# Kernel optimization log

Hardware: AMD Instinct MI355X
Metric: run time of the kernel (lower is better)

The kernel has to match this reference:

```python
import jax, jax.numpy as jnp
import numpy as np

H = 1024      # hidden_dim
S = 32768     # seq_len


def setup_inputs() -> dict:
    key = jax.random.key(0)
    k1, k2, k3, k4, k5 = jax.random.split(key, 5)
    hidden = jax.random.normal(k1, (1, 2 * H), dtype=jnp.float32)
    encoder_output = jax.random.normal(k2, (S, H), dtype=jnp.float32)
    # nn.Linear default init scale ~ 1/sqrt(fan_in)
    attn_w = jax.random.normal(k3, (H, 3 * H), dtype=jnp.float32) / np.sqrt(3 * H)
    attn_b = jax.random.normal(k4, (H,), dtype=jnp.float32) / np.sqrt(3 * H)
    v_w = jax.random.normal(k5, (1, H), dtype=jnp.float32) / np.sqrt(H)
    return {"hidden": hidden, "encoder_output": encoder_output,
            "attn_w": attn_w, "attn_b": attn_b, "v_w": v_w}


def reference(hidden, encoder_output, attn_w, attn_b, v_w):
    seq_len = encoder_output.shape[0]
    h_rep = jnp.broadcast_to(hidden, (seq_len, hidden.shape[1]))  # repeat(seq_len, 1)
    cat = jnp.concatenate([h_rep, encoder_output], axis=1)        # [S, 3H]
    energy = jnp.tanh(cat @ attn_w.T + attn_b)                    # [S, H]
    attention = (energy @ v_w.T).squeeze()                        # [S]
    return jax.nn.softmax(attention, axis=0)
```

## Files before the change

kernel.cpp:

```cpp
#include <hip/hip_runtime.h>
#include <hip/hip_bf16.h>

#define H  1024
#define S  32768
#define H2 2048
#define H3 3072

typedef __attribute__((ext_vector_type(8))) short bf16x8;
typedef __attribute__((ext_vector_type(4))) float f32x4;

__device__ __forceinline__ unsigned short f2bf(float f) {
    unsigned u = __float_as_uint(f);
    u += 0x7fffu + ((u >> 16) & 1u);
    return (unsigned short)(u >> 16);
}

__device__ __forceinline__ unsigned cvt_pk(float lo, float hi) {
    __hip_bfloat162 h = __float22bfloat162_rn(make_float2(lo, hi));
    unsigned u;
    __builtin_memcpy(&u, &h, 4);
    return u;
}

__device__ __forceinline__ float tanh_fast(float x) {
    float e = __expf(2.0f * x);
    return 1.0f - 2.0f / (e + 1.0f);
}

__device__ __forceinline__ void async_copy16(const void* g, void* l) {
    __builtin_amdgcn_global_load_lds(
        (const __attribute__((address_space(1))) unsigned int*)g,
        (__attribute__((address_space(3))) unsigned int*)l,
        16, 0, 0);
}

__global__ void prep_all(const float* __restrict__ enc, const float* __restrict__ attn_w,
                         const float* __restrict__ attn_b, const float* __restrict__ hidden,
                         unsigned short* __restrict__ ebf, unsigned short* __restrict__ w2b,
                         float* __restrict__ dvec, float* __restrict__ logits, int do_enc) {
    int b = blockIdx.x;
    if (b < 32) {
        ((float4*)logits)[b * 256 + threadIdx.x] = (float4){0.f, 0.f, 0.f, 0.f};
        return;
    }
    b -= 32;
    if (do_enc) {
        if (b < 32768) {
            size_t idx4 = (size_t)b * 256 + threadIdx.x;
            float4 f = ((const float4*)enc)[idx4];
            ushort4 u;
            u.x = f2bf(f.x); u.y = f2bf(f.y); u.z = f2bf(f.z); u.w = f2bf(f.w);
            ((ushort4*)ebf)[idx4] = u;
            return;
        }
        b -= 32768;
    }
    if (b < 1024) {
        int idx4 = b * 256 + threadIdx.x;
        int n = idx4 >> 8;
        int c = (idx4 & 255) * 4;
        float4 f = *(const float4*)(attn_w + (size_t)n * H3 + H2 + c);
        ushort4 u;
        u.x = f2bf(f.x); u.y = f2bf(f.y); u.z = f2bf(f.z); u.w = f2bf(f.w);
        *(ushort4*)(w2b + (size_t)n * H + c) = u;
        return;
    }
    b -= 1024;
    int wv = threadIdx.x >> 6, lane = threadIdx.x & 63;
    int row = b * 4 + wv;
    const float* wrow = attn_w + (size_t)row * H3;
    float s = 0.f;
    #pragma unroll
    for (int j = 0; j < 32; ++j) {
        int k = lane + j * 64;
        s += wrow[k] * hidden[k];
    }
    #pragma unroll
    for (int m = 1; m <= 32; m <<= 1) s += __shfl_xor(s, m);
    if (lane == 0) dvec[row] = s + attn_b[row];
}

__device__ __forceinline__ void epilogue(const f32x4 acc[4][4], const float* __restrict__ dvec,
                                         const float* __restrict__ vw, float* __restrict__ logits,
                                         int rowBlock, int colBlock, int waveM, int waveN,
                                         int quad, int l16) {
    float rowsum[4][4];
    #pragma unroll
    for (int mi = 0; mi < 4; ++mi)
        #pragma unroll
        for (int r = 0; r < 4; ++r) rowsum[mi][r] = 0.f;

    #pragma unroll
    for (int ni = 0; ni < 4; ++ni) {
        int colg = colBlock * 128 + waveN * 64 + ni * 16 + l16;
        float dv = dvec[colg];
        float vv = vw[colg];
        #pragma unroll
        for (int mi = 0; mi < 4; ++mi)
            #pragma unroll
            for (int r = 0; r < 4; ++r)
                rowsum[mi][r] += tanh_fast(acc[mi][ni][r] + dv) * vv;
    }

    #pragma unroll
    for (int mi = 0; mi < 4; ++mi)
        #pragma unroll
        for (int r = 0; r < 4; ++r) {
            float s = rowsum[mi][r];
            s += __shfl_xor(s, 1);
            s += __shfl_xor(s, 2);
            s += __shfl_xor(s, 4);
            s += __shfl_xor(s, 8);
            rowsum[mi][r] = s;
        }

    if (l16 == 0) {
        int rbase = rowBlock * 128 + waveM * 64 + quad * 4;
        #pragma unroll
        for (int mi = 0; mi < 4; ++mi)
            #pragma unroll
            for (int r = 0; r < 4; ++r)
                atomicAdd(&logits[rbase + mi * 16 + r], rowsum[mi][r]);
    }
}

__global__ __launch_bounds__(256, 2) void attn_gemm_fast(
        const unsigned short* __restrict__ ebf, const unsigned short* __restrict__ w2b,
        const float* __restrict__ dvec, const float* __restrict__ vw,
        float* __restrict__ logits) {
    __shared__ unsigned short Atile[128 * 64];
    __shared__ unsigned short Btile[128 * 64];

    const int tid = threadIdx.x;
    const int rowBlock = blockIdx.x & 255;
    const int colBlock = blockIdx.x >> 8;

    const int lane = tid & 63;
    const int wv = tid >> 6;
    const int waveM = wv >> 1, waveN = wv & 1;
    const int quad = lane >> 4, l16 = lane & 15;

    f32x4 acc[4][4];
    #pragma unroll
    for (int mi = 0; mi < 4; ++mi)
        #pragma unroll
        for (int ni = 0; ni < 4; ++ni)
            acc[mi][ni] = (f32x4){0.f, 0.f, 0.f, 0.f};

    const size_t aRow0 = (size_t)(rowBlock * 128) * H;
    const size_t bRow0 = (size_t)(colBlock * 128) * H;

    int srow[4], sk[4];
    #pragma unroll
    for (int p = 0; p < 4; ++p) {
        int c = p * 256 + tid;
        srow[p] = c >> 3;
        sk[p] = ((c & 7) ^ (srow[p] & 7)) * 8;
    }

    for (int kt = 0; kt < 16; ++kt) {
        const int k0 = kt * 64;

        #pragma unroll
        for (int p = 0; p < 4; ++p) {
            int c = p * 256 + tid;
            async_copy16(ebf + aRow0 + (size_t)srow[p] * H + k0 + sk[p],
                         (char*)Atile + (size_t)c * 16);
        }
        #pragma unroll
        for (int p = 0; p < 4; ++p) {
            int c = p * 256 + tid;
            async_copy16(w2b + bRow0 + (size_t)srow[p] * H + k0 + sk[p],
                         (char*)Btile + (size_t)c * 16);
        }

        __syncthreads();

        #pragma unroll
        for (int kk = 0; kk < 2; ++kk) {
            const int slot = ((kk * 4 + quad) ^ (l16 & 7)) * 16;
            bf16x8 af[4], bfr[4];
            #pragma unroll
            for (int i = 0; i < 4; ++i) {
                int ar = waveM * 64 + i * 16 + l16;
                int br = waveN * 64 + i * 16 + l16;
                af[i]  = *(const bf16x8*)((const char*)Atile + ar * 128 + slot);
                bfr[i] = *(const bf16x8*)((const char*)Btile + br * 128 + slot);
            }
            #pragma unroll
            for (int mi = 0; mi < 4; ++mi)
                #pragma unroll
                for (int ni = 0; ni < 4; ++ni)
                    acc[mi][ni] = __builtin_amdgcn_mfma_f32_16x16x32_bf16(
                        af[mi], bfr[ni], acc[mi][ni], 0, 0, 0);
        }

        __syncthreads();
    }

    epilogue(acc, dvec, vw, logits, rowBlock, colBlock, waveM, waveN, quad, l16);
}

__global__ __launch_bounds__(256, 2) void attn_gemm_fb(
        const float* __restrict__ enc, const unsigned short* __restrict__ w2b,
        const float* __restrict__ dvec, const float* __restrict__ vw,
        float* __restrict__ logits) {
    __shared__ unsigned short Atile[128 * 32];
    __shared__ unsigned short Btile[128 * 32];

    const int tid = threadIdx.x;
    const int rowBlock = blockIdx.x & 255;
    const int colBlock = blockIdx.x >> 8;

    const int lane = tid & 63;
    const int wv = tid >> 6;
    const int waveM = wv >> 1, waveN = wv & 1;
    const int quad = lane >> 4, l16 = lane & 15;

    f32x4 acc[4][4];
    #pragma unroll
    for (int mi = 0; mi < 4; ++mi)
        #pragma unroll
        for (int ni = 0; ni < 4; ++ni)
            acc[mi][ni] = (f32x4){0.f, 0.f, 0.f, 0.f};

    const int arow = tid >> 3;
    const int akc  = (tid & 7) * 4;
    const size_t encRowBase = (size_t)(rowBlock * 128) * H;

    const unsigned short* Abase = Atile + (waveM * 64 + l16) * 32 + quad * 8;
    const unsigned short* Bbase = Btile + (waveN * 64 + l16) * 32 + quad * 8;

    for (int kt = 0; kt < 32; ++kt) {
        const int k0 = kt * 32;
        #pragma unroll
        for (int p = 0; p < 2; ++p) {
            int c = p * 256 + tid;
            int n = c >> 2, kk = (c & 3) * 8;
            async_copy16(w2b + (size_t)(colBlock * 128 + n) * H + k0 + kk,
                         (char*)Btile + (size_t)c * 16);
        }
        float4 av[4];
        #pragma unroll
        for (int p = 0; p < 4; ++p)
            av[p] = *(const float4*)(enc + encRowBase + (size_t)(arow + p * 32) * H + k0 + akc);
        #pragma unroll
        for (int p = 0; p < 4; ++p) {
            uint2 u;
            u.x = cvt_pk(av[p].x, av[p].y);
            u.y = cvt_pk(av[p].z, av[p].w);
            *(uint2*)(Atile + (arow + p * 32) * 32 + akc) = u;
        }

        __syncthreads();

        bf16x8 af[4], bfr[4];
        #pragma unroll
        for (int i = 0; i < 4; ++i) {
            af[i]  = *(const bf16x8*)(Abase + i * 16 * 32);
            bfr[i] = *(const bf16x8*)(Bbase + i * 16 * 32);
        }
        #pragma unroll
        for (int mi = 0; mi < 4; ++mi)
            #pragma unroll
            for (int ni = 0; ni < 4; ++ni)
                acc[mi][ni] = __builtin_amdgcn_mfma_f32_16x16x32_bf16(
                    af[mi], bfr[ni], acc[mi][ni], 0, 0, 0);

        __syncthreads();
    }

    epilogue(acc, dvec, vw, logits, rowBlock, colBlock, waveM, waveN, quad, l16);
}

__global__ __launch_bounds__(1024) void softmax_k(float* __restrict__ x) {
    __shared__ float red[16];
    const int tid = threadIdx.x;
    const int lane = tid & 63, wv = tid >> 6;

    float v[32];
    float m = -1e30f;
    #pragma unroll
    for (int i = 0; i < 32; ++i) {
        v[i] = x[tid + (i << 10)];
        m = fmaxf(m, v[i]);
    }
    #pragma unroll
    for (int o = 1; o < 64; o <<= 1) m = fmaxf(m, __shfl_xor(m, o));
    if (lane == 0) red[wv] = m;
    __syncthreads();
    #pragma unroll
    for (int i = 0; i < 16; ++i) m = fmaxf(m, red[i]);
    __syncthreads();

    float s = 0.f;
    #pragma unroll
    for (int i = 0; i < 32; ++i) {
        v[i] = expf(v[i] - m);
        s += v[i];
    }
    #pragma unroll
    for (int o = 1; o < 64; o <<= 1) s += __shfl_xor(s, o);
    if (lane == 0) red[wv] = s;
    __syncthreads();
    float tot = 0.f;
    #pragma unroll
    for (int i = 0; i < 16; ++i) tot += red[i];
    float inv = 1.0f / tot;

    #pragma unroll
    for (int i = 0; i < 32; ++i) x[tid + (i << 10)] = v[i] * inv;
}

extern "C" void kernel_launch(void* const* d_in, const int* in_sizes, int n_in,
                              void* d_out, int out_size, void* d_ws, size_t ws_size,
                              hipStream_t stream) {
    const float* hidden = (const float*)d_in[0];
    const float* enc    = (const float*)d_in[1];
    const float* attn_w = (const float*)d_in[2];
    const float* attn_b = (const float*)d_in[3];
    const float* v_w    = (const float*)d_in[4];
    float* out = (float*)d_out;

    const size_t EBF_BYTES = (size_t)S * H * 2;
    const size_t W2_BYTES  = (size_t)H * H * 2;
    const bool fast = ws_size >= EBF_BYTES + W2_BYTES + 4096;

    if (fast) {
        unsigned short* ebf = (unsigned short*)d_ws;
        unsigned short* w2b = (unsigned short*)((char*)d_ws + EBF_BYTES);
        float* dvec = (float*)((char*)d_ws + EBF_BYTES + W2_BYTES);
        prep_all<<<dim3(32 + 32768 + 1024 + 256), dim3(256), 0, stream>>>(
            enc, attn_w, attn_b, hidden, ebf, w2b, dvec, out, 1);
        attn_gemm_fast<<<dim3(2048), dim3(256), 0, stream>>>(ebf, w2b, dvec, v_w, out);
    } else {
        unsigned short* w2b = (unsigned short*)d_ws;
        float* dvec = (float*)((char*)d_ws + W2_BYTES);
        prep_all<<<dim3(32 + 1024 + 256), dim3(256), 0, stream>>>(
            enc, attn_w, attn_b, hidden, nullptr, w2b, dvec, out, 0);
        attn_gemm_fb<<<dim3(2048), dim3(256), 0, stream>>>(enc, w2b, dvec, v_w, out);
    }
    softmax_k<<<dim3(1), dim3(1024), 0, stream>>>(out);
}
```

Baseline: 301.3 us.

## Load fp32 encoder tiles directly via async copy and convert to bf16 in registers

Removes the separate pass that converted the whole encoder output to bf16 in workspace. The GEMM now async-copies fp32 encoder tiles into a swizzled shared buffer and converts them to bf16 when building MFMA fragments. This saves the extra write and re-read of a 64MB bf16 copy. In exchange the GEMM reads twice as many A bytes per tile, which are re-read by all 8 column blocks. Shared memory use grows to 48KB per block and register-side conversion work is added.

```diff
diff --git a/kernel.cpp b/kernel.cpp
--- a/kernel.cpp
+++ b/kernel.cpp
@@ -124,11 +124,11 @@
     }
 }
 
-__global__ __launch_bounds__(256, 2) void attn_gemm_fast(
-        const unsigned short* __restrict__ ebf, const unsigned short* __restrict__ w2b,
+__global__ __launch_bounds__(256, 2) void attn_gemm_f32a(
+        const float* __restrict__ enc, const unsigned short* __restrict__ w2b,
         const float* __restrict__ dvec, const float* __restrict__ vw,
         float* __restrict__ logits) {
-    __shared__ unsigned short Atile[128 * 64];
+    __shared__ float Af[128 * 64];
     __shared__ unsigned short Btile[128 * 64];
 
     const int tid = threadIdx.x;
@@ -150,27 +150,34 @@
     const size_t aRow0 = (size_t)(rowBlock * 128) * H;
     const size_t bRow0 = (size_t)(colBlock * 128) * H;
 
-    int srow[4], sk[4];
+    int srA[8], skA[8];
+    #pragma unroll
+    for (int p = 0; p < 8; ++p) {
+        int c = p * 256 + tid;
+        srA[p] = c >> 4;
+        skA[p] = ((c & 15) ^ ((srA[p] & 7) << 1)) * 4;
+    }
+    int srB[4], skB[4];
     #pragma unroll
     for (int p = 0; p < 4; ++p) {
         int c = p * 256 + tid;
-        srow[p] = c >> 3;
-        sk[p] = ((c & 7) ^ (srow[p] & 7)) * 8;
+        srB[p] = c >> 3;
+        skB[p] = ((c & 7) ^ (srB[p] & 7)) * 8;
     }
 
     for (int kt = 0; kt < 16; ++kt) {
         const int k0 = kt * 64;
 
         #pragma unroll
+        for (int p = 0; p < 8; ++p) {
+            int c = p * 256 + tid;
+            async_copy16(enc + aRow0 + (size_t)srA[p] * H + k0 + skA[p],
+                         (char*)Af + (size_t)c * 16);
+        }
+        #pragma unroll
         for (int p = 0; p < 4; ++p) {
             int c = p * 256 + tid;
-            async_copy16(ebf + aRow0 + (size_t)srow[p] * H + k0 + sk[p],
-                         (char*)Atile + (size_t)c * 16);
-        }
-        #pragma unroll
-        for (int p = 0; p < 4; ++p) {
-            int c = p * 256 + tid;
-            async_copy16(w2b + bRow0 + (size_t)srow[p] * H + k0 + sk[p],
+            async_copy16(w2b + bRow0 + (size_t)srB[p] * H + k0 + skB[p],
                          (char*)Btile + (size_t)c * 16);
         }
 
@@ -178,14 +185,24 @@
 
         #pragma unroll
         for (int kk = 0; kk < 2; ++kk) {
-            const int slot = ((kk * 4 + quad) ^ (l16 & 7)) * 16;
+            const int bslot = ((kk * 4 + quad) ^ (l16 & 7)) * 16;
             bf16x8 af[4], bfr[4];
             #pragma unroll
             for (int i = 0; i < 4; ++i) {
                 int ar = waveM * 64 + i * 16 + l16;
+                int cbase = (kk * 8 + quad * 2) ^ ((ar & 7) << 1);
+                const float* ap = Af + ar * 64 + cbase * 4;
+                float4 lo = ((const float4*)ap)[0];
+                float4 hi = ((const float4*)ap)[1];
+                uint4 u;
+                u.x = cvt_pk(lo.x, lo.y);
+                u.y = cvt_pk(lo.z, lo.w);
+                u.z = cvt_pk(hi.x, hi.y);
+                u.w = cvt_pk(hi.z, hi.w);
+                __builtin_memcpy(&af[i], &u, 16);
+
                 int br = waveN * 64 + i * 16 + l16;
-                af[i]  = *(const bf16x8*)((const char*)Atile + ar * 128 + slot);
-                bfr[i] = *(const bf16x8*)((const char*)Btile + br * 128 + slot);
+                bfr[i] = *(const bf16x8*)((const char*)Btile + br * 128 + bslot);
             }
             #pragma unroll
             for (int mi = 0; mi < 4; ++mi)
@@ -194,78 +211,6 @@
                     acc[mi][ni] = __builtin_amdgcn_mfma_f32_16x16x32_bf16(
                         af[mi], bfr[ni], acc[mi][ni], 0, 0, 0);
         }
-
-        __syncthreads();
-    }
-
-    epilogue(acc, dvec, vw, logits, rowBlock, colBlock, waveM, waveN, quad, l16);
-}
-
-__global__ __launch_bounds__(256, 2) void attn_gemm_fb(
-        const float* __restrict__ enc, const unsigned short* __restrict__ w2b,
-        const float* __restrict__ dvec, const float* __restrict__ vw,
-        float* __restrict__ logits) {
-    __shared__ unsigned short Atile[128 * 32];
-    __shared__ unsigned short Btile[128 * 32];
-
-    const int tid = threadIdx.x;
-    const int rowBlock = blockIdx.x & 255;
-    const int colBlock = blockIdx.x >> 8;
-
-    const int lane = tid & 63;
-    const int wv = tid >> 6;
-    const int waveM = wv >> 1, waveN = wv & 1;
-    const int quad = lane >> 4, l16 = lane & 15;
-
-    f32x4 acc[4][4];
-    #pragma unroll
-    for (int mi = 0; mi < 4; ++mi)
-        #pragma unroll
-        for (int ni = 0; ni < 4; ++ni)
-            acc[mi][ni] = (f32x4){0.f, 0.f, 0.f, 0.f};
-
-    const int arow = tid >> 3;
-    const int akc  = (tid & 7) * 4;
-    const size_t encRowBase = (size_t)(rowBlock * 128) * H;
-
-    const unsigned short* Abase = Atile + (waveM * 64 + l16) * 32 + quad * 8;
-    const unsigned short* Bbase = Btile + (waveN * 64 + l16) * 32 + quad * 8;
-
-    for (int kt = 0; kt < 32; ++kt) {
-        const int k0 = kt * 32;
-        #pragma unroll
-        for (int p = 0; p < 2; ++p) {
-            int c = p * 256 + tid;
-            int n = c >> 2, kk = (c & 3) * 8;
-            async_copy16(w2b + (size_t)(colBlock * 128 + n) * H + k0 + kk,
-                         (char*)Btile + (size_t)c * 16);
-        }
-        float4 av[4];
-        #pragma unroll
-        for (int p = 0; p < 4; ++p)
-            av[p] = *(const float4*)(enc + encRowBase + (size_t)(arow + p * 32) * H + k0 + akc);
-        #pragma unroll
-        for (int p = 0; p < 4; ++p) {
-            uint2 u;
-            u.x = cvt_pk(av[p].x, av[p].y);
-            u.y = cvt_pk(av[p].z, av[p].w);
-            *(uint2*)(Atile + (arow + p * 32) * 32 + akc) = u;
-        }
-
-        __syncthreads();
-
-        bf16x8 af[4], bfr[4];
-        #pragma unroll
-        for (int i = 0; i < 4; ++i) {
-            af[i]  = *(const bf16x8*)(Abase + i * 16 * 32);
-            bfr[i] = *(const bf16x8*)(Bbase + i * 16 * 32);
-        }
-        #pragma unroll
-        for (int mi = 0; mi < 4; ++mi)
-            #pragma unroll
-            for (int ni = 0; ni < 4; ++ni)
-                acc[mi][ni] = __builtin_amdgcn_mfma_f32_16x16x32_bf16(
-                    af[mi], bfr[ni], acc[mi][ni], 0, 0, 0);
 
         __syncthreads();
     }
@@ -322,23 +267,12 @@
     const float* v_w    = (const float*)d_in[4];
     float* out = (float*)d_out;
 
-    const size_t EBF_BYTES = (size_t)S * H * 2;
-    const size_t W2_BYTES  = (size_t)H * H * 2;
-    const bool fast = ws_size >= EBF_BYTES + W2_BYTES + 4096;
-
-    if (fast) {
-        unsigned short* ebf = (unsigned short*)d_ws;
-        unsigned short* w2b = (unsigned short*)((char*)d_ws + EBF_BYTES);
-        float* dvec = (float*)((char*)d_ws + EBF_BYTES + W2_BYTES);
-        prep_all<<<dim3(32 + 32768 + 1024 + 256), dim3(256), 0, stream>>>(
-            enc, attn_w, attn_b, hidden, ebf, w2b, dvec, out, 1);
-        attn_gemm_fast<<<dim3(2048), dim3(256), 0, stream>>>(ebf, w2b, dvec, v_w, out);
-    } else {
-        unsigned short* w2b = (unsigned short*)d_ws;
-        float* dvec = (float*)((char*)d_ws + W2_BYTES);
-        prep_all<<<dim3(32 + 1024 + 256), dim3(256), 0, stream>>>(
-            enc, attn_w, attn_b, hidden, nullptr, w2b, dvec, out, 0);
-        attn_gemm_fb<<<dim3(2048), dim3(256), 0, stream>>>(enc, w2b, dvec, v_w, out);
-    }
+    const size_t W2_BYTES = (size_t)H * H * 2;
+    unsigned short* w2b = (unsigned short*)d_ws;
+    float* dvec = (float*)((char*)d_ws + W2_BYTES);
+
+    prep_all<<<dim3(32 + 1024 + 256), dim3(256), 0, stream>>>(
+        enc, attn_w, attn_b, hidden, nullptr, w2b, dvec, out, 0);
+    attn_gemm_f32a<<<dim3(2048), dim3(256), 0, stream>>>(enc, w2b, dvec, v_w, out);
     softmax_k<<<dim3(1), dim3(1024), 0, stream>>>(out);
 }
```

Result: slower. 336.9 us (+11.8%).
